# Performance work log

Hardware: AMD Instinct MI355X
Metric: run time of the kernel (lower is better)

The kernel has to match this reference:

```python
import jax, jax.numpy as jnp
import numpy as np

N_NODES = 100000
N_EDGES = 1600000
IN_DIM = 128
HIDDEN = 128
N_GRAPHS = 256


def setup_inputs() -> dict:
    key = jax.random.key(0)
    ks = jax.random.split(key, 12)
    x = jax.random.normal(ks[0], (N_NODES, IN_DIM), dtype=jnp.float32)
    edge_index = jax.random.randint(ks[1], (2, N_EDGES), 0, N_NODES, dtype=jnp.int64)
    batch = jnp.sort(jax.random.randint(ks[2], (N_NODES,), 0, N_GRAPHS, dtype=jnp.int64))
    s = 0.05
    W1 = jax.random.normal(ks[3], (IN_DIM, HIDDEN), dtype=jnp.float32) * s
    b1 = jnp.zeros((HIDDEN,), dtype=jnp.float32)
    W2 = jax.random.normal(ks[4], (HIDDEN, HIDDEN), dtype=jnp.float32) * s
    b2 = jnp.zeros((HIDDEN,), dtype=jnp.float32)
    W3 = jax.random.normal(ks[5], (HIDDEN, HIDDEN), dtype=jnp.float32) * s
    b3 = jnp.zeros((HIDDEN,), dtype=jnp.float32)
    Wh = jax.random.normal(ks[6], (HIDDEN, 2), dtype=jnp.float32) * s
    bh = jnp.zeros((2,), dtype=jnp.float32)
    return {"x": x, "edge_index": edge_index, "batch": batch,
            "W1": W1, "b1": b1, "W2": W2, "b2": b2, "W3": W3, "b3": b3,
            "Wh": Wh, "bh": bh}


def _gcn_structure(edge_index, n_nodes):
    # PyG GCNConv default: add self-loops, symmetric deg^-1/2 normalization.
    loop = jnp.arange(n_nodes, dtype=edge_index.dtype)
    src = jnp.concatenate([edge_index[0], loop])  # message source j
    dst = jnp.concatenate([edge_index[1], loop])  # aggregate at i
    deg = jax.ops.segment_sum(jnp.ones_like(dst, dtype=jnp.float32), dst,
                              num_segments=n_nodes)
    dinv = jnp.where(deg > 0, jax.lax.rsqrt(deg), 0.0)
    norm = dinv[src] * dinv[dst]  # [E + N]
    return src, dst, norm


def _gcn_conv(x, W, b, src, dst, norm, n_nodes):
    h = x @ W  # dense transform first (PyG order)
    msg = h[src] * norm[:, None]  # gather + per-edge scale
    agg = jax.ops.segment_sum(msg, dst, num_segments=n_nodes)  # scatter-add
    return agg + b


def reference(x, edge_index, batch, W1, b1, W2, b2, W3, b3, Wh, bh):
    n = x.shape[0]
    src, dst, norm = _gcn_structure(edge_index, n)
    # dropout is a no-op in eval mode (training=False)
    h = jax.nn.relu(_gcn_conv(x, W1, b1, src, dst, norm, n))
    h = jax.nn.relu(_gcn_conv(h, W2, b2, src, dst, norm, n))
    h = jax.nn.relu(_gcn_conv(h, W3, b3, src, dst, norm, n))
    # global_mean_pool over graph ids
    sums = jax.ops.segment_sum(h, batch, num_segments=N_GRAPHS)
    cnts = jax.ops.segment_sum(jnp.ones((n,), dtype=h.dtype), batch,
                               num_segments=N_GRAPHS)
    pooled = sums / jnp.maximum(cnts, 1.0)[:, None]
    return pooled @ Wh + bh  # [N_GRAPHS, 2]
```

## Files before the change

### kernel.cpp

```cpp
#include <hip/hip_runtime.h>


#define D 128
#define NB_SHIFT 8
#define BCAP 8192
#define EPB 16384

typedef unsigned int uint;
typedef unsigned short ushort;
typedef __attribute__((ext_vector_type(8))) short short8;
typedef __attribute__((ext_vector_type(4))) float f32x4;

__device__ __forceinline__ ushort f2bf(float f) {
    uint u = __float_as_uint(f);
    uint r = (u + 0x7fffu + ((u >> 16) & 1u)) >> 16;
    return (ushort)r;
}
__device__ __forceinline__ float bf2f(ushort b) {
    return __uint_as_float(((uint)b) << 16);
}
__device__ __forceinline__ float q15f(uint q) {
    return __uint_as_float(0x30000000u | (q << 13));
}

__device__ __forceinline__ void async_cp16(const ushort* g, ushort* lds_uniform) {
    __builtin_amdgcn_global_load_lds(
        (const __attribute__((address_space(1))) unsigned int*)g,
        (__attribute__((address_space(3))) unsigned int*)lds_uniform,
        16, 0, 0);
}

__global__ __launch_bounds__(256) void k_bucketA(const int* __restrict__ src,
                                                 const int* __restrict__ dst, int E,
                                                 int nbk, int* __restrict__ gcur,
                                                 uint* __restrict__ arena) {
    __shared__ int hist[512];
    __shared__ int rbase[512];
    int t = threadIdx.x;
    int e0 = blockIdx.x * EPB;
    int e1 = min(e0 + EPB, E);
    for (int i = t; i < nbk; i += 256) hist[i] = 0;
    __syncthreads();
    for (int e = e0 + t; e < e1; e += 256)
        atomicAdd(&hist[dst[e] >> NB_SHIFT], 1);
    __syncthreads();
    for (int i = t; i < nbk; i += 256) {
        int c = hist[i];
        rbase[i] = (c > 0) ? atomicAdd(&gcur[i], c) : 0;
        hist[i] = 0;
    }
    __syncthreads();
    for (int e = e0 + t; e < e1; e += 256) {
        int d = dst[e];
        int s = src[e];
        int b = d >> NB_SHIFT;
        int pos = rbase[b] + atomicAdd(&hist[b], 1);
        if (pos < BCAP)
            arena[(size_t)b * BCAP + pos] =
                ((uint)(d & ((1 << NB_SHIFT) - 1)) << 17) | (uint)s;
    }
}

__global__ __launch_bounds__(256) void k_degB(const uint* __restrict__ arena,
                                              const int* __restrict__ gcur, int N,
                                              int* __restrict__ degi,
                                              float* __restrict__ dinv) {
    int b = blockIdx.x;
    int t = threadIdx.x;
    __shared__ int hist[256];
    hist[t] = 0;
    __syncthreads();
    int cnt = min(gcur[b], BCAP);
    const uint* seg = arena + (size_t)b * BCAP;
    for (int i = t; i < cnt; i += 256)
        atomicAdd(&hist[seg[i] >> 17], 1);
    __syncthreads();
    int node = (b << NB_SHIFT) + t;
    if (node < N) {
        int c = hist[t];
        degi[node] = c;
        dinv[node] = rsqrtf((float)(c + 1));
    }
}

__global__ void k_scan1(const int* __restrict__ cnt, int N, int* __restrict__ bsum) {
    __shared__ int sdata[256];
    int t = threadIdx.x;
    int base = blockIdx.x * 1024 + t * 4;
    int s = 0;
#pragma unroll
    for (int j = 0; j < 4; j++) { int i = base + j; if (i < N) s += cnt[i]; }
    sdata[t] = s; __syncthreads();
    for (int off = 128; off > 0; off >>= 1) {
        if (t < off) sdata[t] += sdata[t + off];
        __syncthreads();
    }
    if (t == 0) bsum[blockIdx.x] = sdata[0];
}

__global__ void k_scan2(int* __restrict__ bsum, int nb) {
    if (threadIdx.x == 0) {
        int run = 0;
        for (int b = 0; b < nb; b++) { int v = bsum[b]; bsum[b] = run; run += v; }
    }
}

__global__ void k_scan3(const int* __restrict__ cnt, int N, const int* __restrict__ bofs,
                        int* __restrict__ row_start, int E) {
    __shared__ int sdata[256];
    int t = threadIdx.x;
    int base = blockIdx.x * 1024 + t * 4;
    int v[4]; int s = 0;
#pragma unroll
    for (int j = 0; j < 4; j++) { int i = base + j; v[j] = (i < N) ? cnt[i] : 0; s += v[j]; }
    sdata[t] = s; __syncthreads();
    for (int off = 1; off < 256; off <<= 1) {
        int x = (t >= off) ? sdata[t - off] : 0;
        __syncthreads();
        sdata[t] += x;
        __syncthreads();
    }
    int excl = (t == 0) ? 0 : sdata[t - 1];
    int run = bofs[blockIdx.x] + excl;
#pragma unroll
    for (int j = 0; j < 4; j++) {
        int i = base + j;
        if (i < N) row_start[i] = run;
        run += v[j];
    }
    if (blockIdx.x == 0 && t == 0) row_start[N] = E;
}

__global__ __launch_bounds__(256) void k_bucketB(const uint* __restrict__ arena,
                                                 const int* __restrict__ gcur,
                                                 const int* __restrict__ row_start,
                                                 const float* __restrict__ dinv,
                                                 int N, uint* __restrict__ csr) {
    int b = blockIdx.x;
    int t = threadIdx.x;
    int n0 = b << NB_SHIFT;
    int nn = min(1 << NB_SHIFT, N - n0);
    __shared__ float sdinv[256];
    __shared__ int sstart[256];
    __shared__ int scur[256];
    __shared__ uint sout[BCAP];
    for (int i = t; i < nn; i += 256) {
        sdinv[i]  = dinv[n0 + i];
        sstart[i] = row_start[n0 + i];
        scur[i]   = 0;
    }
    __syncthreads();
    int cnt = min(gcur[b], BCAP);
    int csr0 = sstart[0];
    for (int i = t; i < cnt; i += 256) {
        uint en = arena[(size_t)b * BCAP + i];
        int dl = en >> 17;
        int s  = en & 0x1FFFF;
        float nrm = dinv[s] * sdinv[dl];
        uint q = ((__float_as_uint(nrm) + 0x1000u) >> 13) & 0x7FFFu;
        int pos = atomicAdd(&scur[dl], 1);
        sout[(sstart[dl] - csr0) + pos] = ((uint)s << 15) | q;
    }
    __syncthreads();
    for (int i = t; i < cnt; i += 256)
        csr[csr0 + i] = sout[i];
}

__global__ void k_wsplit(const float* __restrict__ W, ushort* __restrict__ Wf) {
    int idx = blockIdx.x * blockDim.x + threadIdx.x;
    if (idx >= 32768) return;
    int i  = idx & 7;
    int l  = (idx >> 3) & 63;
    int nt = (idx >> 9) & 7;
    int kt = (idx >> 12) & 3;
    int h  = idx >> 14;
    int k = kt * 32 + (l >> 4) * 8 + i;
    int n = nt * 16 + (l & 15);
    float w = W[k * D + n];
    ushort hi = f2bf(w);
    ushort v = (h == 0) ? hi : f2bf(w - bf2f(hi));
    Wf[idx] = v;
}

template <bool AF32>
__global__ __launch_bounds__(256) void k_gemm(const void* __restrict__ Ain,
                                              const ushort* __restrict__ Wf,
                                              ushort* __restrict__ out, int N) {
    __shared__ ushort As[64 * D];
    int t = threadIdx.x;
    int rowb = blockIdx.x * 64;

    if (AF32) {
        const float* A = (const float*)Ain;
#pragma unroll
        for (int i = 0; i < 8; i++) {
            int u = i * 256 + t;
            int row = u >> 5, c4 = u & 31;
            int grow = rowb + row;
            float4 v = make_float4(0.f, 0.f, 0.f, 0.f);
            if (grow < N) v = *(const float4*)(A + (size_t)grow * D + c4 * 4);
            uint2 p;
            p.x = (uint)f2bf(v.x) | ((uint)f2bf(v.y) << 16);
            p.y = (uint)f2bf(v.z) | ((uint)f2bf(v.w) << 16);
            int byteoff = row * 256 + ((c4 * 8) ^ ((row & 7) << 4));
            *(uint2*)((char*)As + byteoff) = p;
        }
    } else {
        const ushort* A = (const ushort*)Ain;
#pragma unroll
        for (int i = 0; i < 4; i++) {
            int u = i * 256 + t;
            int row = u >> 4, cp = u & 15;
            int grow = rowb + row;
            if (grow >= N) grow = N - 1;
            int gc = cp ^ (row & 7);
            const ushort* gp = A + (size_t)grow * D + gc * 8;
            ushort* lb = As + (size_t)(i * 256 + (t & 192)) * 8;
            async_cp16(gp, lb);
        }
        asm volatile("s_waitcnt vmcnt(0)" ::: "memory");
    }
    __syncthreads();

    int wave = t >> 6, lane = t & 63;
    const short8* Wf8 = (const short8*)Wf;

    short8 bhi[2][4], blo[2][4];
#pragma unroll
    for (int j = 0; j < 2; j++) {
        int nt = wave * 2 + j;
#pragma unroll
        for (int kt = 0; kt < 4; kt++) {
            bhi[j][kt] = Wf8[(size_t)((0 * 4 + kt) * 8 + nt) * 64 + lane];
            blo[j][kt] = Wf8[(size_t)((1 * 4 + kt) * 8 + nt) * 64 + lane];
        }
    }

    f32x4 acc[4][2];
#pragma unroll
    for (int m = 0; m < 4; m++)
#pragma unroll
        for (int j = 0; j < 2; j++) acc[m][j] = (f32x4){0.f, 0.f, 0.f, 0.f};

#pragma unroll
    for (int m = 0; m < 4; m++) {
        int r = m * 16 + (lane & 15);
#pragma unroll
        for (int kt = 0; kt < 4; kt++) {
            int raw = kt * 64 + (lane >> 4) * 16;
            short8 a = *(const short8*)((const char*)As + r * 256 + (raw ^ ((r & 7) << 4)));
#pragma unroll
            for (int j = 0; j < 2; j++) {
                acc[m][j] = __builtin_amdgcn_mfma_f32_16x16x32_bf16(a, bhi[j][kt], acc[m][j], 0, 0, 0);
                acc[m][j] = __builtin_amdgcn_mfma_f32_16x16x32_bf16(a, blo[j][kt], acc[m][j], 0, 0, 0);
            }
        }
    }

#pragma unroll
    for (int m = 0; m < 4; m++) {
#pragma unroll
        for (int j = 0; j < 2; j++) {
            int colb = (wave * 2 + j) * 16 + (lane & 15);
#pragma unroll
            for (int jj = 0; jj < 4; jj++) {
                int grow = rowb + m * 16 + (lane >> 4) * 4 + jj;
                if (grow < N)
                    out[(size_t)grow * D + colb] = f2bf(acc[m][j][jj]);
            }
        }
    }
}

__device__ __forceinline__ void agg_core(const ushort* __restrict__ T,
                                         const uint* __restrict__ csr,
                                         float di, int beg, int end, int col,
                                         float& a0, float& a1) {
    int lane = threadIdx.x & 63;
    for (int e = beg; e < end; e += 16) {
        int li = e + (lane & 15);
        uint myc = csr[li < end ? li : end - 1];
        uint v[16];
        float nn[16];
#pragma unroll
        for (int q = 0; q < 16; q++) {
            uint c = __builtin_amdgcn_readlane(myc, q);
            nn[q] = (e + q < end) ? q15f(c & 0x7FFFu) : 0.f;
            v[q] = *(const uint*)(T + (size_t)(c >> 15) * D + col);
        }
#pragma unroll
        for (int q = 0; q < 16; q++) {
            a0 = fmaf(nn[q], __uint_as_float(v[q] << 16), a0);
            a1 = fmaf(nn[q], __uint_as_float(v[q] & 0xffff0000u), a1);
        }
    }
}

__global__ __launch_bounds__(256) void k_agg(const ushort* __restrict__ T,
                                             const float* __restrict__ dinv,
                                             const int* __restrict__ row_start,
                                             const uint* __restrict__ csr,
                                             const float* __restrict__ bias,
                                             ushort* __restrict__ out, int N) {
    int node = __builtin_amdgcn_readfirstlane(blockIdx.x * 4 + (threadIdx.x >> 6));
    if (node >= N) return;
    int lane = threadIdx.x & 63;
    int col = lane * 2;

    float di = dinv[node];
    uint vs = *(const uint*)(T + (size_t)node * D + col);
    float sw = di * di;
    float a0 = sw * __uint_as_float(vs << 16);
    float a1 = sw * __uint_as_float(vs & 0xffff0000u);

    agg_core(T, csr, di, row_start[node], row_start[node + 1], col, a0, a1);

    a0 = fmaxf(a0 + bias[col], 0.f);
    a1 = fmaxf(a1 + bias[col + 1], 0.f);
    ushort2 o; o.x = f2bf(a0); o.y = f2bf(a1);
    *(ushort2*)(out + (size_t)node * D + col) = o;
}

__global__ __launch_bounds__(256) void k_agg_head(const ushort* __restrict__ T,
                                                  const float* __restrict__ dinv,
                                                  const int* __restrict__ row_start,
                                                  const uint* __restrict__ csr,
                                                  const float* __restrict__ bias,
                                                  const float* __restrict__ Wh,
                                                  float2* __restrict__ y, int N) {
    int node = __builtin_amdgcn_readfirstlane(blockIdx.x * 4 + (threadIdx.x >> 6));
    if (node >= N) return;
    int lane = threadIdx.x & 63;
    int col = lane * 2;

    float di = dinv[node];
    uint vs = *(const uint*)(T + (size_t)node * D + col);
    float sw = di * di;
    float a0 = sw * __uint_as_float(vs << 16);
    float a1 = sw * __uint_as_float(vs & 0xffff0000u);

    agg_core(T, csr, di, row_start[node], row_start[node + 1], col, a0, a1);

    a0 = fmaxf(a0 + bias[col], 0.f);
    a1 = fmaxf(a1 + bias[col + 1], 0.f);

    float p0 = a0 * Wh[col * 2 + 0] + a1 * Wh[(col + 1) * 2 + 0];
    float p1 = a0 * Wh[col * 2 + 1] + a1 * Wh[(col + 1) * 2 + 1];
#pragma unroll
    for (int off = 32; off > 0; off >>= 1) {
        p0 += __shfl_xor(p0, off);
        p1 += __shfl_xor(p1, off);
    }
    if (lane == 0) y[node] = make_float2(p0, p1);
}

__global__ __launch_bounds__(256) void k_pool2(const float2* __restrict__ y,
                                               const int* __restrict__ batch, int N,
                                               const float* __restrict__ bh,
                                               float* __restrict__ out) {
    int g = blockIdx.x;
    int t = threadIdx.x;
    int lo = 0, hi = N;
    while (lo < hi) { int m = (lo + hi) >> 1; if (batch[m] < g) lo = m + 1; else hi = m; }
    int beg = lo;
    lo = 0; hi = N;
    while (lo < hi) { int m = (lo + hi) >> 1; if (batch[m] < g + 1) lo = m + 1; else hi = m; }
    int endi = lo;

    float s0 = 0.f, s1 = 0.f;
    for (int i = beg + t; i < endi; i += 256) {
        float2 v = y[i];
        s0 += v.x; s1 += v.y;
    }
    __shared__ float r0[256], r1[256];
    r0[t] = s0; r1[t] = s1;
    __syncthreads();
    for (int off = 128; off > 0; off >>= 1) {
        if (t < off) { r0[t] += r0[t + off]; r1[t] += r1[t + off]; }
        __syncthreads();
    }
    if (t == 0) {
        float cnt = (float)((endi - beg) > 0 ? (endi - beg) : 1);
        out[g * 2 + 0] = r0[0] / cnt + bh[0];
        out[g * 2 + 1] = r1[0] / cnt + bh[1];
    }
}

extern "C" void kernel_launch(void* const* d_in, const int* in_sizes, int n_in,
                              void* d_out, int out_size, void* d_ws, size_t ws_size,
                              hipStream_t stream) {
    const float* x   = (const float*)d_in[0];
    const int* eidx  = (const int*)d_in[1];
    const int* batch = (const int*)d_in[2];
    const float* W1 = (const float*)d_in[3];
    const float* b1 = (const float*)d_in[4];
    const float* W2 = (const float*)d_in[5];
    const float* b2 = (const float*)d_in[6];
    const float* W3 = (const float*)d_in[7];
    const float* b3 = (const float*)d_in[8];
    const float* Wh = (const float*)d_in[9];
    const float* bh = (const float*)d_in[10];

    int E = in_sizes[1] / 2;
    int N = in_sizes[2];
    int ngraphs = out_size / 2;
    const int* src = eidx;
    const int* dst = eidx + E;
    int nbk = (N + (1 << NB_SHIFT) - 1) >> NB_SHIFT;

    char* ws = (char*)d_ws;
    size_t off = 0;
    auto alloc = [&](size_t bytes) -> void* {
        void* p = ws + off;
        off = (off + bytes + 255) & ~(size_t)255;
        return p;
    };
    ushort* Hbf      = (ushort*)alloc((size_t)N * D * 2);
    ushort* T        = (ushort*)alloc((size_t)N * D * 2);
    ushort* Wf1      = (ushort*)alloc(32768 * 2);
    ushort* Wf2      = (ushort*)alloc(32768 * 2);
    ushort* Wf3      = (ushort*)alloc(32768 * 2);
    int*    degi     = (int*)alloc((size_t)N * 4);
    float*  dinv     = (float*)alloc((size_t)N * 4);
    int*    row_start= (int*)alloc((size_t)(N + 1) * 4);
    int*    gcur     = (int*)alloc((size_t)nbk * 4);
    int*    bofs     = (int*)alloc(4096);
    float2* y        = (float2*)alloc((size_t)N * 8);
    uint*   csr      = (uint*)alloc((size_t)E * 4);
    uint*   arena    = (uint*)alloc((size_t)nbk * BCAP * 4);
    (void)ws_size;

    hipMemsetAsync(gcur, 0, (size_t)nbk * 4, stream);

    k_bucketA<<<(E + EPB - 1) / EPB, 256, 0, stream>>>(src, dst, E, nbk, gcur, arena);
    k_degB<<<nbk, 256, 0, stream>>>(arena, gcur, N, degi, dinv);

    int nb = (N + 1023) / 1024;
    k_scan1<<<nb, 256, 0, stream>>>(degi, N, bofs);
    k_scan2<<<1, 64, 0, stream>>>(bofs, nb);
    k_scan3<<<nb, 256, 0, stream>>>(degi, N, bofs, row_start, E);

    k_bucketB<<<nbk, 256, 0, stream>>>(arena, gcur, row_start, dinv, N, csr);

    k_wsplit<<<128, 256, 0, stream>>>(W1, Wf1);
    k_wsplit<<<128, 256, 0, stream>>>(W2, Wf2);
    k_wsplit<<<128, 256, 0, stream>>>(W3, Wf3);

    int gemm_grid = (N + 63) / 64;
    int agg_grid = (N + 3) / 4;

    k_gemm<true><<<gemm_grid, 256, 0, stream>>>(x, Wf1, T, N);
    k_agg<<<agg_grid, 256, 0, stream>>>(T, dinv, row_start, csr, b1, Hbf, N);
    k_gemm<false><<<gemm_grid, 256, 0, stream>>>(Hbf, Wf2, T, N);
    k_agg<<<agg_grid, 256, 0, stream>>>(T, dinv, row_start, csr, b2, Hbf, N);
    k_gemm<false><<<gemm_grid, 256, 0, stream>>>(Hbf, Wf3, T, N);
    k_agg_head<<<agg_grid, 256, 0, stream>>>(T, dinv, row_start, csr, b3, Wh, y, N);
    k_pool2<<<ngraphs, 256, 0, stream>>>(y, batch, N, bh, (float*)d_out);
}
```

Before: 337.7 us.

## Prefetch next CSR chunk in aggregation, merge weight-split launches, shrink bucket EPB

The aggregation loop now loads the next 16 CSR entries while it processes the current chunk, so the index load latency overlaps the feature gathers. The three weight-split kernels are merged into one launch that writes a contiguous buffer, which saves two launches. EPB drops from 16384 to 4096, so the bucketing kernel runs with more blocks. These changes are unrelated, and the prefetch costs extra registers in the aggregation kernels.

```diff
diff --git a/kernel.cpp b/kernel.cpp
--- a/kernel.cpp
+++ b/kernel.cpp
@@ -4,7 +4,7 @@
 #define D 128
 #define NB_SHIFT 8
 #define BCAP 8192
-#define EPB 16384
+#define EPB 4096
 
 typedef unsigned int uint;
 typedef unsigned short ushort;
@@ -166,9 +166,13 @@
         csr[csr0 + i] = sout[i];
 }
 
-__global__ void k_wsplit(const float* __restrict__ W, ushort* __restrict__ Wf) {
-    int idx = blockIdx.x * blockDim.x + threadIdx.x;
-    if (idx >= 32768) return;
+__global__ void k_wsplit3(const float* __restrict__ W1, const float* __restrict__ W2,
+                          const float* __restrict__ W3, ushort* __restrict__ Wf) {
+    int gidx = blockIdx.x * blockDim.x + threadIdx.x;
+    if (gidx >= 3 * 32768) return;
+    int which = gidx >> 15;
+    int idx = gidx & 32767;
+    const float* W = (which == 0) ? W1 : (which == 1) ? W2 : W3;
     int i  = idx & 7;
     int l  = (idx >> 3) & 63;
     int nt = (idx >> 9) & 7;
@@ -179,7 +183,7 @@
     float w = W[k * D + n];
     ushort hi = f2bf(w);
     ushort v = (h == 0) ? hi : f2bf(w - bf2f(hi));
-    Wf[idx] = v;
+    Wf[gidx] = v;
 }
 
 template <bool AF32>
@@ -274,17 +278,20 @@
 
 __device__ __forceinline__ void agg_core(const ushort* __restrict__ T,
                                          const uint* __restrict__ csr,
-                                         float di, int beg, int end, int col,
+                                         int beg, int end, int col,
                                          float& a0, float& a1) {
-    int lane = threadIdx.x & 63;
+    if (beg >= end) return;
+    int lane16 = threadIdx.x & 15;
+    uint cur = csr[min(beg + lane16, end - 1)];
     for (int e = beg; e < end; e += 16) {
-        int li = e + (lane & 15);
-        uint myc = csr[li < end ? li : end - 1];
+        uint nxt = 0;
+        int en = e + 16;
+        if (en < end) nxt = csr[min(en + lane16, end - 1)];
         uint v[16];
         float nn[16];
 #pragma unroll
         for (int q = 0; q < 16; q++) {
-            uint c = __builtin_amdgcn_readlane(myc, q);
+            uint c = __builtin_amdgcn_readlane(cur, q);
             nn[q] = (e + q < end) ? q15f(c & 0x7FFFu) : 0.f;
             v[q] = *(const uint*)(T + (size_t)(c >> 15) * D + col);
         }
@@ -293,6 +300,7 @@
             a0 = fmaf(nn[q], __uint_as_float(v[q] << 16), a0);
             a1 = fmaf(nn[q], __uint_as_float(v[q] & 0xffff0000u), a1);
         }
+        cur = nxt;
     }
 }
 
@@ -313,7 +321,7 @@
     float a0 = sw * __uint_as_float(vs << 16);
     float a1 = sw * __uint_as_float(vs & 0xffff0000u);
 
-    agg_core(T, csr, di, row_start[node], row_start[node + 1], col, a0, a1);
+    agg_core(T, csr, row_start[node], row_start[node + 1], col, a0, a1);
 
     a0 = fmaxf(a0 + bias[col], 0.f);
     a1 = fmaxf(a1 + bias[col + 1], 0.f);
@@ -339,7 +347,7 @@
     float a0 = sw * __uint_as_float(vs << 16);
     float a1 = sw * __uint_as_float(vs & 0xffff0000u);
 
-    agg_core(T, csr, di, row_start[node], row_start[node + 1], col, a0, a1);
+    agg_core(T, csr, row_start[node], row_start[node + 1], col, a0, a1);
 
     a0 = fmaxf(a0 + bias[col], 0.f);
     a1 = fmaxf(a1 + bias[col + 1], 0.f);
@@ -417,9 +425,7 @@
     };
     ushort* Hbf      = (ushort*)alloc((size_t)N * D * 2);
     ushort* T        = (ushort*)alloc((size_t)N * D * 2);
-    ushort* Wf1      = (ushort*)alloc(32768 * 2);
-    ushort* Wf2      = (ushort*)alloc(32768 * 2);
-    ushort* Wf3      = (ushort*)alloc(32768 * 2);
+    ushort* Wf       = (ushort*)alloc(3 * 32768 * 2);
     int*    degi     = (int*)alloc((size_t)N * 4);
     float*  dinv     = (float*)alloc((size_t)N * 4);
     int*    row_start= (int*)alloc((size_t)(N + 1) * 4);
@@ -442,18 +448,16 @@
 
     k_bucketB<<<nbk, 256, 0, stream>>>(arena, gcur, row_start, dinv, N, csr);
 
-    k_wsplit<<<128, 256, 0, stream>>>(W1, Wf1);
-    k_wsplit<<<128, 256, 0, stream>>>(W2, Wf2);
-    k_wsplit<<<128, 256, 0, stream>>>(W3, Wf3);
+    k_wsplit3<<<384, 256, 0, stream>>>(W1, W2, W3, Wf);
 
     int gemm_grid = (N + 63) / 64;
     int agg_grid = (N + 3) / 4;
 
-    k_gemm<true><<<gemm_grid, 256, 0, stream>>>(x, Wf1, T, N);
+    k_gemm<true><<<gemm_grid, 256, 0, stream>>>(x, Wf, T, N);
     k_agg<<<agg_grid, 256, 0, stream>>>(T, dinv, row_start, csr, b1, Hbf, N);
-    k_gemm<false><<<gemm_grid, 256, 0, stream>>>(Hbf, Wf2, T, N);
+    k_gemm<false><<<gemm_grid, 256, 0, stream>>>(Hbf, Wf + 32768, T, N);
     k_agg<<<agg_grid, 256, 0, stream>>>(T, dinv, row_start, csr, b2, Hbf, N);
-    k_gemm<false><<<gemm_grid, 256, 0, stream>>>(Hbf, Wf3, T, N);
+    k_gemm<false><<<gemm_grid, 256, 0, stream>>>(Hbf, Wf + 65536, T, N);
     k_agg_head<<<agg_grid, 256, 0, stream>>>(T, dinv, row_start, csr, b3, Wh, y, N);
     k_pool2<<<ngraphs, 256, 0, stream>>>(y, batch, N, bh, (float*)d_out);
 }
```

Result: faster. 307.9 us (-8.8%).
